# Optimization experiments

Hardware: AMD Instinct MI355X
Metric: run time of the kernel (lower is better)

## Reference

```python
import jax, jax.numpy as jnp
import numpy as np
from jax import lax

B, T, H = 32768, 64, 16
VOCAB_USER = 600001
VOCAB_LAUNCH = 3


def setup_inputs() -> dict:
    key = jax.random.key(0)
    ks = jax.random.split(key, 10)
    s = 1.0 / np.sqrt(H)
    return {
        "user_id": jax.random.randint(ks[0], (B,), 0, VOCAB_USER),
        "launch_seq": jax.random.randint(ks[1], (B, T), 0, VOCAB_LAUNCH),
        "user_emb": jax.random.normal(ks[2], (VOCAB_USER, H), dtype=jnp.float32),
        "launch_emb": jax.random.normal(ks[3], (VOCAB_LAUNCH, H), dtype=jnp.float32),
        "W_ih": jax.random.uniform(ks[4], (3 * H, H), jnp.float32, -s, s),
        "W_hh": jax.random.uniform(ks[5], (3 * H, H), jnp.float32, -s, s),
        "b_ih": jax.random.uniform(ks[6], (3 * H,), jnp.float32, -s, s),
        "b_hh": jax.random.uniform(ks[7], (3 * H,), jnp.float32, -s, s),
        "fc_W": jax.random.uniform(ks[8], (1, 2 * H), jnp.float32, -s, s),
        "fc_b": jax.random.uniform(ks[9], (1,), jnp.float32, -s, s),
    }


def reference(user_id, launch_seq, user_emb, launch_emb, W_ih, W_hh, b_ih, b_hh, fc_W, fc_b):
    u = user_emb[user_id]                      # (B, H)
    x = launch_emb[launch_seq]                 # (B, T, H)
    # precompute input contributions to the gates for all timesteps
    gx_all = jnp.einsum('bth,gh->btg', x, W_ih) + b_ih  # (B, T, 3H)

    def step(h, gx):
        gh = h @ W_hh.T + b_hh                 # (B, 3H)
        r = jax.nn.sigmoid(gx[:, :H] + gh[:, :H])
        z = jax.nn.sigmoid(gx[:, H:2 * H] + gh[:, H:2 * H])
        n = jnp.tanh(gx[:, 2 * H:] + r * gh[:, 2 * H:])
        h_new = (1.0 - z) * n + z * h
        return h_new, h_new

    h0 = jnp.zeros((x.shape[0], H), dtype=x.dtype)
    _, hs = lax.scan(step, h0, jnp.swapaxes(gx_all, 0, 1))  # hs: (T, B, H)
    pooled = jnp.mean(hs, axis=0)              # (B, H)
    fc_in = jnp.concatenate([u, pooled], axis=1)  # (B, 2H)
    return fc_in @ fc_W.T + fc_b               # (B, 1)
```

## Files before the change

kernel.cpp:

```cpp
#include <hip/hip_runtime.h>
#include <hip/hip_bf16.h>
#include <string.h>


#define NBLK 2048

typedef __attribute__((ext_vector_type(8))) short    short8;
typedef __attribute__((ext_vector_type(4))) float    floatx4;
typedef __attribute__((ext_vector_type(4))) unsigned uintx4;

static __device__ __forceinline__ float fexp2(float x) { return __builtin_amdgcn_exp2f(x); }
static __device__ __forceinline__ float frcp(float x)  { return __builtin_amdgcn_rcpf(x); }
static __device__ __forceinline__ unsigned f2u(float f) { unsigned u; memcpy(&u, &f, 4); return u; }
static __device__ __forceinline__ unsigned short bfrne(float f) {
    union { __hip_bfloat16 b; unsigned short u; } cv; cv.b = __float2bfloat16(f); return cv.u;
}
static __device__ __forceinline__ float bf2f(unsigned short u) {
    unsigned v = ((unsigned)u) << 16; float f; memcpy(&f, &v, 4); return f;
}
static __device__ __forceinline__ unsigned pkrnd(float a, float b) {
    unsigned ua = f2u(a) + 0x8000u;
    unsigned ub = f2u(b) + 0x8000u;
    return __builtin_amdgcn_perm(ub, ua, 0x07060302u);
}
static __device__ __forceinline__ float sel3f(int c, float a0, float a1, float a2) {
    return c == 0 ? a0 : (c == 1 ? a1 : a2);
}
static __device__ __forceinline__ unsigned sel3u(int c, unsigned a0, unsigned a1, unsigned a2) {
    return c == 0 ? a0 : (c == 1 ? a1 : a2);
}

__global__ __launch_bounds__(64) void gru16(
    const int* __restrict__ user_id,
    const int* __restrict__ launch_seq,
    const float* __restrict__ user_emb,
    const float* __restrict__ launch_emb,
    const float* __restrict__ W_ih,
    const float* __restrict__ W_hh,
    const float* __restrict__ b_ih,
    const float* __restrict__ b_hh,
    const float* __restrict__ fc_W,
    const float* __restrict__ fc_b,
    float* __restrict__ out)
{
    constexpr float L  = 1.4426950408889634f;
    constexpr float L2 = 2.8853900817779268f;
    constexpr unsigned K_LO = 0x3F80u;
    constexpr unsigned K_HI = 0x3F800000u;

    __shared__ float gxlut[144];

    const int tid  = threadIdx.x;
    const int col  = tid & 15;
    const int quad = tid >> 4;
    const bool isq2 = (quad == 2);
    const long long sampBase = (long long)blockIdx.x * 16;

    unsigned pk[4];
    {
        const int* sp = launch_seq + (sampBase + col) * 64;
        #pragma unroll
        for (int w = 0; w < 4; ++w) {
            unsigned p = 0;
            #pragma unroll
            for (int j = 0; j < 4; ++j) {
                int4 v = ((const int4*)sp)[w * 4 + j];
                p |= ((unsigned)v.x & 3u) << (2 * (4 * j + 0));
                p |= ((unsigned)v.y & 3u) << (2 * (4 * j + 1));
                p |= ((unsigned)v.z & 3u) << (2 * (4 * j + 2));
                p |= ((unsigned)v.w & 3u) << (2 * (4 * j + 3));
            }
            pk[w] = p;
        }
    }

    for (int idx = tid; idx < 144; idx += 64) {
        int s = idx / 48, g = idx - s * 48;
        float dot = b_ih[g];
        #pragma unroll
        for (int k = 0; k < 16; ++k)
            dot = fmaf(W_ih[g * 16 + k], launch_emb[s * 16 + k], dot);
        int gate = g >> 4, dim = g & 15;
        gxlut[(gate * 3 + s) * 16 + dim] =
            (g < 32) ? (-L * (dot + b_hh[g])) : (L2 * dot);
    }

    __syncthreads();

    short8 Ar, Az, An_;
    {
        auto pack8 = [&](const float* w) {
            uintx4 hi;
            #pragma unroll
            for (int p = 0; p < 4; ++p)
                hi[p] = (unsigned)bfrne(w[2 * p]) | ((unsigned)bfrne(w[2 * p + 1]) << 16);
            return __builtin_bit_cast(short8, hi);
        };
        auto makeA = [&](int grow, float scale, const float* gx3, float bias, short8& A) {
            float w[8];
            #pragma unroll
            for (int j = 0; j < 8; ++j) w[j] = 0.f;
            if (quad < 2) {
                const float* row = W_hh + (grow + col) * 16 + quad * 8;
                float4 a = *(const float4*)row;
                float4 b = *(const float4*)(row + 4);
                w[0] = scale * a.x; w[1] = scale * a.y; w[2] = scale * a.z; w[3] = scale * a.w;
                w[4] = scale * b.x; w[5] = scale * b.y; w[6] = scale * b.z; w[7] = scale * b.w;
            } else if (quad == 2) {
                if (gx3) {
                    #pragma unroll
                    for (int c = 0; c < 3; ++c) {
                        float g = gx3[c * 16 + col];
                        w[c] = g;
                        w[3 + c] = g - bf2f(bfrne(g));
                    }
                } else {
                    w[6] = bias;
                    w[7] = bias - bf2f(bfrne(bias));
                }
            }
            A = pack8(w);
        };
        makeA(0,  -L, &gxlut[0],       0.f,               Ar);
        makeA(16, -L, &gxlut[3 * 16],  0.f,               Az);
        makeA(32,  L2, (const float*)0, L2 * b_hh[32 + col], An_);
    }

    floatx4 gn0 = *(const floatx4*)&gxlut[(6 + 0) * 16 + quad * 4];
    floatx4 gn1 = *(const floatx4*)&gxlut[(6 + 1) * 16 + quad * 4];
    floatx4 gn2 = *(const floatx4*)&gxlut[(6 + 2) * 16 + quad * 4];

    const int a_lo = (col + 32 * (quad & 1)) * 4;
    const int a_hi = a_lo + 64;

    floatx4 h    = {0.f, 0.f, 0.f, 0.f};
    floatx4 pool = {0.f, 0.f, 0.f, 0.f};
    const floatx4 CZ = {0.f, 0.f, 0.f, 0.f};

    short8 B;
    {
        int c0 = (int)(pk[0] & 3u);
        uintx4 b = {0u, 0u, 0u, 0u};
        if (isq2) {
            b[0] = sel3u(c0, K_LO, K_HI, 0u);
            b[1] = sel3u(c0, K_HI, 0u, K_LO);
            b[2] = sel3u(c0, 0u, K_LO, K_HI);
            b[3] = K_LO | K_HI;
        }
        B = __builtin_bit_cast(short8, b);
    }

    #pragma unroll
    for (int w = 0; w < 4; ++w) {
        unsigned cw  = pk[w];
        unsigned ncw = (pk[w] >> 2) | (w < 3 ? (pk[w + 1] << 30) : 0u);
        #pragma unroll 4
        for (int tt = 0; tt < 16; ++tt) {
            int c = (int)(cw & 3u);

            floatx4 dr = __builtin_amdgcn_mfma_f32_16x16x32_bf16(Ar,  B, CZ, 0, 0, 0);
            floatx4 dz = __builtin_amdgcn_mfma_f32_16x16x32_bf16(Az,  B, CZ, 0, 0, 0);
            floatx4 dn = __builtin_amdgcn_mfma_f32_16x16x32_bf16(An_, B, CZ, 0, 0, 0);

            #pragma unroll
            for (int e = 0; e < 4; ++e) {
                float er = fexp2(dr[e]);
                float ez = fexp2(dz[e]);
                float t1 = 1.0f + er;
                float t2 = 1.0f + ez;
                float rp = frcp(t1 * t2);
                float r  = rp * t2;
                float z  = rp * t1;
                float gn = sel3f(c, gn0[e], gn1[e], gn2[e]);
                float y  = fmaf(r, dn[e], gn);
                float nn = fmaf(-2.0f, frcp(1.0f + fexp2(y)), 1.0f);
                h[e] = fmaf(z, h[e] - nn, nn);
                pool[e] += h[e];
            }

            unsigned hp0 = pkrnd(h[0], h[1]);
            unsigned hp1 = pkrnd(h[2], h[3]);
            int cn = (int)(ncw & 3u);
            uintx4 b;
            b[0] = (unsigned)__builtin_amdgcn_ds_bpermute(a_lo, (int)hp0);
            b[1] = (unsigned)__builtin_amdgcn_ds_bpermute(a_lo, (int)hp1);
            b[2] = (unsigned)__builtin_amdgcn_ds_bpermute(a_hi, (int)hp0);
            b[3] = (unsigned)__builtin_amdgcn_ds_bpermute(a_hi, (int)hp1);
            unsigned oh0 = sel3u(cn, K_LO, K_HI, 0u);
            unsigned oh1 = sel3u(cn, K_HI, 0u, K_LO);
            unsigned oh2 = sel3u(cn, 0u, K_LO, K_HI);
            b[0] = isq2 ? oh0 : b[0];
            b[1] = isq2 ? oh1 : b[1];
            b[2] = isq2 ? oh2 : b[2];
            b[3] = isq2 ? (K_LO | K_HI) : b[3];
            B = __builtin_bit_cast(short8, b);
            cw >>= 2;
            ncw >>= 2;
        }
    }

    float4 f1 = *(const float4*)&fc_W[quad * 4];
    float4 f2 = *(const float4*)&fc_W[16 + quad * 4];
    int uid = user_id[sampBase + col];
    float4 uu = *(const float4*)&user_emb[(long long)uid * 16 + quad * 4];
    const float inv64 = 1.0f / 64.0f;
    float val = f1.x * uu.x + f1.y * uu.y + f1.z * uu.z + f1.w * uu.w;
    val = fmaf(f2.x * inv64, pool[0], val);
    val = fmaf(f2.y * inv64, pool[1], val);
    val = fmaf(f2.z * inv64, pool[2], val);
    val = fmaf(f2.w * inv64, pool[3], val);
    val += __shfl_xor(val, 16);
    val += __shfl_xor(val, 32);
    if (quad == 0) out[sampBase + col] = val + fc_b[0];
}

extern "C" void kernel_launch(void* const* d_in, const int* in_sizes, int n_in,
                              void* d_out, int out_size, void* d_ws, size_t ws_size,
                              hipStream_t stream) {
    const int*   user_id    = (const int*)d_in[0];
    const int*   launch_seq = (const int*)d_in[1];
    const float* user_emb   = (const float*)d_in[2];
    const float* launch_emb = (const float*)d_in[3];
    const float* W_ih       = (const float*)d_in[4];
    const float* W_hh       = (const float*)d_in[5];
    const float* b_ih       = (const float*)d_in[6];
    const float* b_hh       = (const float*)d_in[7];
    const float* fc_W       = (const float*)d_in[8];
    const float* fc_b       = (const float*)d_in[9];
    float* out = (float*)d_out;

    gru16<<<dim3(NBLK), dim3(64), 0, stream>>>(
        user_id, launch_seq, user_emb, launch_emb,
        W_ih, W_hh, b_ih, b_hh, fc_W, fc_b, out);
}
```

Before: 133.7 us.

## Switch GRU recurrence MFMA to fp16 16x16x16 and drop per-step lane permutes

Replaces the bf16 16x16x32 MFMA, which folded the one-hot input gate terms and hi/lo bias splits into extra K rows, with fp16 16x16x16 MFMA over just the hidden state. Input gate contributions are now added in VALU through per-token selects, and the n-gate bias goes into the accumulator. The new B operand layout matches the MFMA output layout, so the four ds_bpermute calls and the one-hot packing each step are removed and h is packed in place with cvt_pkrtz. The trade-off is fp16 round-toward-zero precision for h and weights, plus a few more VALU selects and adds per step.

```diff
diff --git a/kernel.cpp b/kernel.cpp
--- a/kernel.cpp
+++ b/kernel.cpp
@@ -5,32 +5,20 @@
 
 #define NBLK 2048
 
-typedef __attribute__((ext_vector_type(8))) short    short8;
+typedef __attribute__((ext_vector_type(4))) _Float16 half4v;
 typedef __attribute__((ext_vector_type(4))) float    floatx4;
-typedef __attribute__((ext_vector_type(4))) unsigned uintx4;
+typedef __attribute__((ext_vector_type(2))) unsigned uintx2;
 
 static __device__ __forceinline__ float fexp2(float x) { return __builtin_amdgcn_exp2f(x); }
 static __device__ __forceinline__ float frcp(float x)  { return __builtin_amdgcn_rcpf(x); }
-static __device__ __forceinline__ unsigned f2u(float f) { unsigned u; memcpy(&u, &f, 4); return u; }
-static __device__ __forceinline__ unsigned short bfrne(float f) {
-    union { __hip_bfloat16 b; unsigned short u; } cv; cv.b = __float2bfloat16(f); return cv.u;
-}
-static __device__ __forceinline__ float bf2f(unsigned short u) {
-    unsigned v = ((unsigned)u) << 16; float f; memcpy(&f, &v, 4); return f;
-}
-static __device__ __forceinline__ unsigned pkrnd(float a, float b) {
-    unsigned ua = f2u(a) + 0x8000u;
-    unsigned ub = f2u(b) + 0x8000u;
-    return __builtin_amdgcn_perm(ub, ua, 0x07060302u);
+static __device__ __forceinline__ unsigned pkh2(float a, float b) {
+    return __builtin_bit_cast(unsigned, __builtin_amdgcn_cvt_pkrtz(a, b));
 }
 static __device__ __forceinline__ float sel3f(int c, float a0, float a1, float a2) {
     return c == 0 ? a0 : (c == 1 ? a1 : a2);
 }
-static __device__ __forceinline__ unsigned sel3u(int c, unsigned a0, unsigned a1, unsigned a2) {
-    return c == 0 ? a0 : (c == 1 ? a1 : a2);
-}
 
-__global__ __launch_bounds__(64) void gru16(
+__global__ __launch_bounds__(64) void gru16h(
     const int* __restrict__ user_id,
     const int* __restrict__ launch_seq,
     const float* __restrict__ user_emb,
@@ -45,15 +33,12 @@
 {
     constexpr float L  = 1.4426950408889634f;
     constexpr float L2 = 2.8853900817779268f;
-    constexpr unsigned K_LO = 0x3F80u;
-    constexpr unsigned K_HI = 0x3F800000u;
 
     __shared__ float gxlut[144];
 
     const int tid  = threadIdx.x;
     const int col  = tid & 15;
     const int quad = tid >> 4;
-    const bool isq2 = (quad == 2);
     const long long sampBase = (long long)blockIdx.x * 16;
 
     unsigned pk[4];
@@ -85,117 +70,79 @@
             (g < 32) ? (-L * (dot + b_hh[g])) : (L2 * dot);
     }
 
+    half4v Ar, Az, An_;
+    {
+        auto makeA = [&](int grow, float scale) {
+            const float* row = W_hh + (grow + col) * 16 + quad * 4;
+            float4 a = *(const float4*)row;
+            half4v r;
+            r[0] = (_Float16)(scale * a.x);
+            r[1] = (_Float16)(scale * a.y);
+            r[2] = (_Float16)(scale * a.z);
+            r[3] = (_Float16)(scale * a.w);
+            return r;
+        };
+        Ar  = makeA(0,  -L);
+        Az  = makeA(16, -L);
+        An_ = makeA(32,  L2);
+    }
+
+    floatx4 Cn;
+    {
+        float4 b = *(const float4*)&b_hh[32 + quad * 4];
+        Cn = floatx4{L2 * b.x, L2 * b.y, L2 * b.z, L2 * b.w};
+    }
+
     __syncthreads();
 
-    short8 Ar, Az, An_;
-    {
-        auto pack8 = [&](const float* w) {
-            uintx4 hi;
-            #pragma unroll
-            for (int p = 0; p < 4; ++p)
-                hi[p] = (unsigned)bfrne(w[2 * p]) | ((unsigned)bfrne(w[2 * p + 1]) << 16);
-            return __builtin_bit_cast(short8, hi);
-        };
-        auto makeA = [&](int grow, float scale, const float* gx3, float bias, short8& A) {
-            float w[8];
-            #pragma unroll
-            for (int j = 0; j < 8; ++j) w[j] = 0.f;
-            if (quad < 2) {
-                const float* row = W_hh + (grow + col) * 16 + quad * 8;
-                float4 a = *(const float4*)row;
-                float4 b = *(const float4*)(row + 4);
-                w[0] = scale * a.x; w[1] = scale * a.y; w[2] = scale * a.z; w[3] = scale * a.w;
-                w[4] = scale * b.x; w[5] = scale * b.y; w[6] = scale * b.z; w[7] = scale * b.w;
-            } else if (quad == 2) {
-                if (gx3) {
-                    #pragma unroll
-                    for (int c = 0; c < 3; ++c) {
-                        float g = gx3[c * 16 + col];
-                        w[c] = g;
-                        w[3 + c] = g - bf2f(bfrne(g));
-                    }
-                } else {
-                    w[6] = bias;
-                    w[7] = bias - bf2f(bfrne(bias));
-                }
-            }
-            A = pack8(w);
-        };
-        makeA(0,  -L, &gxlut[0],       0.f,               Ar);
-        makeA(16, -L, &gxlut[3 * 16],  0.f,               Az);
-        makeA(32,  L2, (const float*)0, L2 * b_hh[32 + col], An_);
-    }
-
-    floatx4 gn0 = *(const floatx4*)&gxlut[(6 + 0) * 16 + quad * 4];
-    floatx4 gn1 = *(const floatx4*)&gxlut[(6 + 1) * 16 + quad * 4];
-    floatx4 gn2 = *(const floatx4*)&gxlut[(6 + 2) * 16 + quad * 4];
-
-    const int a_lo = (col + 32 * (quad & 1)) * 4;
-    const int a_hi = a_lo + 64;
+    floatx4 gr0 = *(const floatx4*)&gxlut[(0 * 3 + 0) * 16 + quad * 4];
+    floatx4 gr1 = *(const floatx4*)&gxlut[(0 * 3 + 1) * 16 + quad * 4];
+    floatx4 gr2 = *(const floatx4*)&gxlut[(0 * 3 + 2) * 16 + quad * 4];
+    floatx4 gz0 = *(const floatx4*)&gxlut[(1 * 3 + 0) * 16 + quad * 4];
+    floatx4 gz1 = *(const floatx4*)&gxlut[(1 * 3 + 1) * 16 + quad * 4];
+    floatx4 gz2 = *(const floatx4*)&gxlut[(1 * 3 + 2) * 16 + quad * 4];
+    floatx4 gn0 = *(const floatx4*)&gxlut[(2 * 3 + 0) * 16 + quad * 4];
+    floatx4 gn1 = *(const floatx4*)&gxlut[(2 * 3 + 1) * 16 + quad * 4];
+    floatx4 gn2 = *(const floatx4*)&gxlut[(2 * 3 + 2) * 16 + quad * 4];
 
     floatx4 h    = {0.f, 0.f, 0.f, 0.f};
     floatx4 pool = {0.f, 0.f, 0.f, 0.f};
     const floatx4 CZ = {0.f, 0.f, 0.f, 0.f};
-
-    short8 B;
-    {
-        int c0 = (int)(pk[0] & 3u);
-        uintx4 b = {0u, 0u, 0u, 0u};
-        if (isq2) {
-            b[0] = sel3u(c0, K_LO, K_HI, 0u);
-            b[1] = sel3u(c0, K_HI, 0u, K_LO);
-            b[2] = sel3u(c0, 0u, K_LO, K_HI);
-            b[3] = K_LO | K_HI;
-        }
-        B = __builtin_bit_cast(short8, b);
-    }
+    uintx2 Bb = {0u, 0u};
 
     #pragma unroll
     for (int w = 0; w < 4; ++w) {
-        unsigned cw  = pk[w];
-        unsigned ncw = (pk[w] >> 2) | (w < 3 ? (pk[w + 1] << 30) : 0u);
+        unsigned cw = pk[w];
         #pragma unroll 4
         for (int tt = 0; tt < 16; ++tt) {
             int c = (int)(cw & 3u);
+            cw >>= 2;
 
-            floatx4 dr = __builtin_amdgcn_mfma_f32_16x16x32_bf16(Ar,  B, CZ, 0, 0, 0);
-            floatx4 dz = __builtin_amdgcn_mfma_f32_16x16x32_bf16(Az,  B, CZ, 0, 0, 0);
-            floatx4 dn = __builtin_amdgcn_mfma_f32_16x16x32_bf16(An_, B, CZ, 0, 0, 0);
+            half4v B = __builtin_bit_cast(half4v, Bb);
+            floatx4 dr = __builtin_amdgcn_mfma_f32_16x16x16f16(Ar,  B, CZ, 0, 0, 0);
+            floatx4 dz = __builtin_amdgcn_mfma_f32_16x16x16f16(Az,  B, CZ, 0, 0, 0);
+            floatx4 dn = __builtin_amdgcn_mfma_f32_16x16x16f16(An_, B, Cn, 0, 0, 0);
 
             #pragma unroll
             for (int e = 0; e < 4; ++e) {
-                float er = fexp2(dr[e]);
-                float ez = fexp2(dz[e]);
+                float ar = dr[e] + sel3f(c, gr0[e], gr1[e], gr2[e]);
+                float az = dz[e] + sel3f(c, gz0[e], gz1[e], gz2[e]);
+                float gn = sel3f(c, gn0[e], gn1[e], gn2[e]);
+                float er = fexp2(ar);
+                float ez = fexp2(az);
                 float t1 = 1.0f + er;
                 float t2 = 1.0f + ez;
                 float rp = frcp(t1 * t2);
                 float r  = rp * t2;
                 float z  = rp * t1;
-                float gn = sel3f(c, gn0[e], gn1[e], gn2[e]);
                 float y  = fmaf(r, dn[e], gn);
                 float nn = fmaf(-2.0f, frcp(1.0f + fexp2(y)), 1.0f);
                 h[e] = fmaf(z, h[e] - nn, nn);
                 pool[e] += h[e];
             }
 
-            unsigned hp0 = pkrnd(h[0], h[1]);
-            unsigned hp1 = pkrnd(h[2], h[3]);
-            int cn = (int)(ncw & 3u);
-            uintx4 b;
-            b[0] = (unsigned)__builtin_amdgcn_ds_bpermute(a_lo, (int)hp0);
-            b[1] = (unsigned)__builtin_amdgcn_ds_bpermute(a_lo, (int)hp1);
-            b[2] = (unsigned)__builtin_amdgcn_ds_bpermute(a_hi, (int)hp0);
-            b[3] = (unsigned)__builtin_amdgcn_ds_bpermute(a_hi, (int)hp1);
-            unsigned oh0 = sel3u(cn, K_LO, K_HI, 0u);
-            unsigned oh1 = sel3u(cn, K_HI, 0u, K_LO);
-            unsigned oh2 = sel3u(cn, 0u, K_LO, K_HI);
-            b[0] = isq2 ? oh0 : b[0];
-            b[1] = isq2 ? oh1 : b[1];
-            b[2] = isq2 ? oh2 : b[2];
-            b[3] = isq2 ? (K_LO | K_HI) : b[3];
-            B = __builtin_bit_cast(short8, b);
-            cw >>= 2;
-            ncw >>= 2;
+            Bb[0] = pkh2(h[0], h[1]);
+            Bb[1] = pkh2(h[2], h[3]);
         }
     }
 
@@ -229,7 +176,7 @@
     const float* fc_b       = (const float*)d_in[9];
     float* out = (float*)d_out;
 
-    gru16<<<dim3(NBLK), dim3(64), 0, stream>>>(
+    gru16h<<<dim3(NBLK), dim3(64), 0, stream>>>(
         user_id, launch_seq, user_emb, launch_emb,
         W_ih, W_hh, b_ih, b_hh, fc_W, fc_b, out);
 }
```

Result: faster. 131.0 us (-2.0%).
